# Performance work log

Measured on AMD Instinct MI355X. Metric: run time of the kernel, lower is better.

## Reference

```python
import jax, jax.numpy as jnp
import numpy as np

B, S, D = 2, 2048, 4096
NH, NKV = 32, 8
HD = D // NH          # 128
NREP = NH // NKV      # 4
SCALE = HD ** -0.5


def setup_inputs() -> dict:
    key = jax.random.key(0)
    kx, kq, kk, kv, ko = jax.random.split(key, 5)
    s = 0.02
    return {
        "x": jax.random.normal(kx, (B, S, D), dtype=jnp.float32),
        "wq": jax.random.normal(kq, (D, NH * HD), dtype=jnp.float32) * s,
        "wk": jax.random.normal(kk, (D, NKV * HD), dtype=jnp.float32) * s,
        "wv": jax.random.normal(kv, (D, NKV * HD), dtype=jnp.float32) * s,
        "wo": jax.random.normal(ko, (NH * HD, D), dtype=jnp.float32) * s,
    }


def reference(x, wq, wk, wv, wo):
    b, s, _ = x.shape
    q = (x @ wq).reshape(b, s, NH, HD)    # b s h d
    k = (x @ wk).reshape(b, s, NKV, HD)   # b s kv d
    v = (x @ wv).reshape(b, s, NKV, HD)
    # GQA: repeat kv heads to match query heads
    k = jnp.repeat(k, NREP, axis=2)       # b s h d
    v = jnp.repeat(v, NREP, axis=2)
    scores = jnp.einsum("bihd,bjhd->bhij", q, k) * SCALE  # b h i j
    causal = jnp.tril(jnp.ones((s, s), dtype=bool))
    scores = jnp.where(causal, scores, jnp.finfo(scores.dtype).min)
    attn = jax.nn.softmax(scores, axis=-1)
    out = jnp.einsum("bhij,bjhd->bihd", attn, v)          # b s h d
    out = out.reshape(b, s, NH * HD)
    return out @ wo
```

## Files before the change

kernel.cpp:

```cpp
#include <hip/hip_runtime.h>
#include <cstdint>
#include <cstddef>

typedef __bf16 bf16x8 __attribute__((ext_vector_type(8)));
typedef float  f32x4  __attribute__((ext_vector_type(4)));
typedef unsigned short u16;

#define SCALE_F 0.08838834764831845f
#define QSCALE_F (0.08838834764831845f * 1.4426950408889634f)

__device__ __forceinline__ u16 f2bf(float f) {
  unsigned int u = __builtin_bit_cast(unsigned int, f);
  u += 0x7fffu + ((u >> 16) & 1u);
  return (u16)(u >> 16);
}

__device__ __forceinline__ unsigned cvt_pk_bf16(float lo, float hi) {
  unsigned r;
  asm("v_cvt_pk_bf16_f32 %0, %1, %2" : "=v"(r) : "v"(lo), "v"(hi));
  return r;
}

__device__ __forceinline__ void load_lds16(const void* g, void* l) {
  __builtin_amdgcn_global_load_lds((const __attribute__((address_space(1))) void*)g,
                                   (__attribute__((address_space(3))) void*)l,
                                   16, 0, 0);
}

__global__ __launch_bounds__(256) void prep_all(const float* __restrict__ x,
                                                const float* __restrict__ wq,
                                                const float* __restrict__ wk,
                                                const float* __restrict__ wv,
                                                const float* __restrict__ wo,
                                                u16* __restrict__ xb,
                                                u16* __restrict__ wqkvT,
                                                u16* __restrict__ woT) {
  __shared__ float tile[64][33];
  const int tid = threadIdx.x;
  int blk = blockIdx.x;
  if (blk < 2048) {
    int idx = blk * 256 + tid;
    const int n4 = 4096 * 4096 / 4;
    for (; idx < n4; idx += 2048 * 256) {
      float4 v = ((const float4*)x)[idx];
      uint2 pk;
      pk.x = (unsigned)f2bf(v.x) | ((unsigned)f2bf(v.y) << 16);
      pk.y = (unsigned)f2bf(v.z) | ((unsigned)f2bf(v.w) << 16);
      ((uint2*)xb)[idx] = pk;
    }
    return;
  }
  blk -= 2048;
  const float* in; u16* out; long C; int nbx; float scale;
  if (blk < 8192)       { in = wq; out = wqkvT;                            C = 4096; nbx = 128; scale = QSCALE_F; }
  else if (blk < 10240) { blk -= 8192;  in = wk; out = wqkvT + (size_t)4096 * 4096; C = 1024; nbx = 32; scale = 1.f; }
  else if (blk < 12288) { blk -= 10240; in = wv; out = wqkvT + (size_t)5120 * 4096; C = 1024; nbx = 32; scale = 1.f; }
  else                  { blk -= 12288; in = wo; out = woT;                C = 4096; nbx = 128; scale = 1.f; }
  const long R = 4096;
  const long c0 = (long)(blk % nbx) * 32, r0 = (long)(blk / nbx) * 64;
  {
    const int tx = tid & 31, ty = tid >> 5;
#pragma unroll
    for (int i = 0; i < 8; i++)
      tile[ty + i * 8][tx] = in[(r0 + ty + i * 8) * C + c0 + tx];
  }
  __syncthreads();
  {
    const int tx = tid & 31, cy = tid >> 5;
#pragma unroll
    for (int i = 0; i < 4; i++) {
      int col = cy + i * 8;
      unsigned val = (unsigned)f2bf(tile[2 * tx][col] * scale) |
                     ((unsigned)f2bf(tile[2 * tx + 1][col] * scale) << 16);
      *(unsigned*)&out[(c0 + col) * R + r0 + 2 * tx] = val;
    }
  }
}

__global__ __launch_bounds__(256) void transpose_u16(const u16* __restrict__ in,
                                                     u16* __restrict__ out,
                                                     int R, int C, int ldi, int ldo) {
  __shared__ u16 tile[32][33];
  const int tx = threadIdx.x, ty = threadIdx.y;
  const long c0 = (long)blockIdx.x * 32, r0 = (long)blockIdx.y * 32;
#pragma unroll
  for (int i = 0; i < 4; i++)
    tile[ty + i * 8][tx] = in[(r0 + ty + i * 8) * (long)ldi + c0 + tx];
  __syncthreads();
#pragma unroll
  for (int i = 0; i < 4; i++)
    out[(c0 + ty + i * 8) * (long)ldo + r0 + tx] = tile[tx][ty + i * 8];
}

#define STGA(db, ks, KC) { int kc_ = (KC) < K ? (KC) : 0; \
    load_lds16(gA0 + kc_, &SA[db][ks][s0 * 8]); \
    load_lds16(gA1 + kc_, &SA[db][ks][s1 * 8]); }
#define STGB(db, ks, KC) { int kc_ = (KC) < K ? (KC) : 0; \
    load_lds16(gB0 + kc_, &SB[db][ks][s0 * 8]); \
    load_lds16(gB1 + kc_, &SB[db][ks][s1 * 8]); }

#define PH(MBc, AU, BU, DBn, KSn, MBn, AN, RDB, BN_, STG, DOVM) { \
    STG; \
    if (DOVM) asm volatile("s_waitcnt vmcnt(8)"); \
    __builtin_amdgcn_s_barrier(); \
    _Pragma("unroll") for (int mm = 0; mm < 4; mm++) \
      AN[mm] = *(const bf16x8*)(&SA[DBn][KSn][aoff + (MBn + mm) * 512]); \
    if (RDB) { \
      _Pragma("unroll") for (int n = 0; n < 4; n++) \
        BN_[n] = *(const bf16x8*)(&SB[DBn][KSn][boff + n * 512]); \
    } \
    __builtin_amdgcn_s_setprio(1); \
    _Pragma("unroll") for (int mm = 0; mm < 4; mm++) \
      _Pragma("unroll") for (int n = 0; n < 4; n++) \
        acc[MBc + mm][n] = __builtin_amdgcn_mfma_f32_16x16x32_bf16(AU[mm], BU[n], acc[MBc + mm][n], 0, 0, 0); \
    __builtin_amdgcn_s_setprio(0); \
  }

template <int BF16_OUT>
__device__ __forceinline__ void gemm_body(const u16* __restrict__ A,
                                          const u16* __restrict__ Bt,
                                          void* __restrict__ Cv,
                                          int M, int N, int K, int NBX) {
  __shared__ u16 SA[2][2][8192];
  __shared__ u16 SB[2][2][8192];
  const int tid = threadIdx.x;
  const int lane = tid & 63;
  const int g = lane >> 4, r16 = lane & 15;
  const int wid = tid >> 6;
  const int wm = wid >> 2, wn = wid & 3;

  const int cpx = gridDim.x >> 3;
  const int lin = (blockIdx.x & 7) * cpx + (blockIdx.x >> 3);
  const long bm = (long)(lin / NBX) * 256;
  const long bn = (long)(lin % NBX) * 256;

  const int s0 = tid, s1 = 512 + tid;
  const int rp0 = s0 >> 3, ci0 = (s0 & 7) ^ (rp0 & 7);
  const int rp1 = s1 >> 3, ci1 = (s1 & 7) ^ (rp1 & 7);
  const long gr0 = rp0 * 2 + (ci0 >> 2), gc0 = (ci0 & 3) * 8;
  const long gr1 = rp1 * 2 + (ci1 >> 2), gc1 = (ci1 & 3) * 8;
  const u16* gA0 = A + (bm + gr0) * K + gc0;
  const u16* gA1 = A + (bm + gr1) * K + gc1;
  const u16* gB0 = Bt + (bn + gr0) * K + gc0;
  const u16* gB1 = Bt + (bn + gr1) * K + gc1;

  const int rA = wm * 128 + r16;
  const int aoff = (rA >> 1) * 64 + ((((rA & 1) << 2) + g) ^ ((rA >> 1) & 7)) * 8;
  const int rB = wn * 64 + r16;
  const int boff = (rB >> 1) * 64 + ((((rB & 1) << 2) + g) ^ ((rB >> 1) & 7)) * 8;

  f32x4 acc[8][4];
#pragma unroll
  for (int m = 0; m < 8; m++)
#pragma unroll
    for (int n = 0; n < 4; n++)
#pragma unroll
      for (int j = 0; j < 4; j++) acc[m][n][j] = 0.f;

  bf16x8 afrX[4], afrY[4], bfrX[4], bfrY[4];

  STGA(0, 0, 0); STGB(0, 0, 0);
  STGA(0, 1, 32); STGB(0, 1, 32);
  STGA(1, 0, 64); STGB(1, 0, 64);
  __builtin_amdgcn_sched_barrier(0);
  asm volatile("s_waitcnt vmcnt(0)" ::: "memory");
  __builtin_amdgcn_s_barrier();

#pragma unroll
  for (int mm = 0; mm < 4; mm++)
    afrX[mm] = *(const bf16x8*)(&SA[0][0][aoff + mm * 512]);
#pragma unroll
  for (int n = 0; n < 4; n++)
    bfrX[n] = *(const bf16x8*)(&SB[0][0][boff + n * 512]);

  for (int it = 0; it < K / 128; it++) {
    const int t0 = it * 128;
    PH(0, afrX, bfrX, 0, 0, 4, afrY, 0, bfrY, STGA(1, 1, t0 + 96), 0);
    PH(4, afrY, bfrX, 0, 1, 0, afrX, 1, bfrY, STGB(1, 1, t0 + 96), 1);
    PH(0, afrX, bfrY, 0, 1, 4, afrY, 0, bfrX, STGA(0, 0, t0 + 128), 0);
    PH(4, afrY, bfrY, 1, 0, 0, afrX, 1, bfrX, STGB(0, 0, t0 + 128), 1);
    PH(0, afrX, bfrX, 1, 0, 4, afrY, 0, bfrY, STGA(0, 1, t0 + 160), 0);
    PH(4, afrY, bfrX, 1, 1, 0, afrX, 1, bfrY, STGB(0, 1, t0 + 160), 1);
    PH(0, afrX, bfrY, 1, 1, 4, afrY, 0, bfrX, STGA(1, 0, t0 + 192), 0);
    PH(4, afrY, bfrY, 0, 0, 0, afrX, 1, bfrX, STGB(1, 0, t0 + 192), 1);
  }

  const long crow = bm + wm * 128 + g * 4;
  const long ccol = bn + wn * 64 + r16;
  if (BF16_OUT) {
    u16* C = (u16*)Cv;
#pragma unroll
    for (int m = 0; m < 8; m++)
#pragma unroll
      for (int n = 0; n < 4; n++)
#pragma unroll
        for (int j = 0; j < 4; j++)
          C[(crow + m * 16 + j) * (long)N + ccol + n * 16] = f2bf(acc[m][n][j]);
  } else {
    float* C = (float*)Cv;
#pragma unroll
    for (int m = 0; m < 8; m++)
#pragma unroll
      for (int n = 0; n < 4; n++)
#pragma unroll
        for (int j = 0; j < 4; j++)
          C[(crow + m * 16 + j) * (long)N + ccol + n * 16] = acc[m][n][j];
  }
}

__global__ __launch_bounds__(512, 2) void gemm_qkv(const u16* __restrict__ A,
                                                   const u16* __restrict__ Bt,
                                                   void* __restrict__ Cv,
                                                   int M, int N, int K, int NBX) {
  gemm_body<1>(A, Bt, Cv, M, N, K, NBX);
}
__global__ __launch_bounds__(512, 2) void gemm_wo(const u16* __restrict__ A,
                                                  const u16* __restrict__ Bt,
                                                  void* __restrict__ Cv,
                                                  int M, int N, int K, int NBX) {
  gemm_body<0>(A, Bt, Cv, M, N, K, NBX);
}

__global__ __launch_bounds__(512, 4) void attn_fwd(const u16* __restrict__ QK,
                                                   const u16* __restrict__ VT,
                                                   u16* __restrict__ Og) {
  __shared__ u16 Ks[2][64 * 128];
  __shared__ u16 Vs[2][128 * 64];
  __shared__ u16 Ps[8][16 * 64];
  const int tid = threadIdx.x;
  const int lane = tid & 63;
  const int w = tid >> 6;
  const int g = lane >> 4, r16 = lane & 15;

  const int lin = (blockIdx.x & 7) * 64 + (blockIdx.x >> 3);
  const int b = lin >> 8;
  const int rem = lin & 255;
  const int kvh = rem >> 5;
  const int hrep = (rem & 31) >> 3;
  const int qtA = rem & 7;
  const int qtB = 15 - qtA;
  const int h = kvh * 4 + hrep;

  const u16* kcol   = QK + (long)b * 2048 * 6144 + 4096 + kvh * 128;
  const u16* vb_ptr = VT + (long)kvh * 128 * 4096 + (long)b * 2048;
  u16* pw = Ps[w];

  const int nktA = 2 * (qtA + 1);
  const int ntot = 34;

  int qbase = qtA * 128;
  int qlo = qbase + w * 16;
  int qrow = qlo + r16;

  bf16x8 qf[4];
  auto load_q = [&]() {
    const u16* qp = QK + ((long)(b * 2048 + qrow)) * 6144 + h * 128 + g * 8;
#pragma unroll
    for (int kc = 0; kc < 4; kc++) qf[kc] = *(const bf16x8*)(qp + kc * 32);
  };
  load_q();

  f32x4 oacc[8];
  float mrun, lrun;
  auto reinit = [&]() {
#pragma unroll
    for (int dt = 0; dt < 8; dt++)
#pragma unroll
      for (int j = 0; j < 4; j++) oacc[dt][j] = 0.f;
    mrun = -__builtin_inff();
    lrun = 0.f;
  };
  reinit();

  auto finalize = [&]() {
    float li[4];
#pragma unroll
    for (int j = 0; j < 4; j++)
      li[j] = 1.f / __shfl(lrun, (lane & 48) + g * 4 + j);
    u16* op = Og + ((long)(b * 2048 + qbase + w * 16 + g * 4)) * 4096 + h * 128 + r16;
#pragma unroll
    for (int dt = 0; dt < 8; dt++)
#pragma unroll
      for (int j = 0; j < 4; j++)
        op[(long)j * 4096 + dt * 16] = f2bf(oacc[dt][j] * li[j]);
  };

  auto stage = [&](int bf, int kb) {
#pragma unroll
    for (int i = 0; i < 2; i++) {
      int slot = i * 512 + tid;
      int r = slot >> 4, cs = slot & 15;
      int ck = (cs & 8) | ((cs ^ r) & 7);
      load_lds16(kcol + (long)(kb + r) * 6144 + ck * 8, &Ks[bf][slot * 8]);
      int d = slot >> 3, c8 = slot & 7;
      int cv = (c8 ^ d) & 7;
      load_lds16(vb_ptr + (long)d * 4096 + kb + cv * 8, &Vs[bf][slot * 8]);
    }
  };

  stage(0, 0);
  __syncthreads();
  int cur = 0;

  for (int i = 0; i < ntot; i++) {
    if (i == nktA) {
      finalize();
      qbase = qtB * 128;
      qlo = qbase + w * 16;
      qrow = qlo + r16;
      load_q();
      reinit();
    }
    const int kt = (i < nktA) ? i : i - nktA;
    const int kb = kt * 64;
    if (i + 1 < ntot) {
      const int ktn = (i + 1 < nktA) ? i + 1 : i + 1 - nktA;
      stage(cur ^ 1, ktn * 64);
    }

    if (kb <= qlo + 15) {
      const bool masked = (kb + 63 > qlo);

      f32x4 st[4];
#pragma unroll
      for (int t = 0; t < 4; t++)
#pragma unroll
        for (int j = 0; j < 4; j++) st[t][j] = 0.f;
#pragma unroll
      for (int t = 0; t < 4; t++) {
        const int r = t * 16 + r16;
#pragma unroll
        for (int kc = 0; kc < 4; kc++) {
          int c = kc * 4 + g;
          int cz = (c & 8) | ((c ^ r) & 7);
          bf16x8 kf = *(const bf16x8*)(&Ks[cur][r * 128 + cz * 8]);
          st[t] = __builtin_amdgcn_mfma_f32_16x16x32_bf16(kf, qf[kc], st[t], 0, 0, 0);
        }
      }

      float p[4][4];
      float tmax = -__builtin_inff();
#pragma unroll
      for (int t = 0; t < 4; t++)
#pragma unroll
        for (int j = 0; j < 4; j++) {
          float s = st[t][j];
          if (masked) {
            int kv = kb + t * 16 + g * 4 + j;
            s = (kv > qrow) ? -__builtin_inff() : s;
          }
          p[t][j] = s;
          tmax = fmaxf(tmax, s);
        }
      tmax = fmaxf(tmax, __shfl_xor(tmax, 16));
      tmax = fmaxf(tmax, __shfl_xor(tmax, 32));

      if (!__all(tmax <= mrun + 8.f)) {
        const float mnew = fmaxf(mrun, tmax);
        const float esc = exp2f(mrun - mnew);
        float es[4];
#pragma unroll
        for (int j = 0; j < 4; j++) es[j] = __shfl(esc, (lane & 48) + g * 4 + j);
#pragma unroll
        for (int dt = 0; dt < 8; dt++)
#pragma unroll
          for (int j = 0; j < 4; j++) oacc[dt][j] *= es[j];
        lrun *= esc;
        mrun = mnew;
      }
      float psum = 0.f;
#pragma unroll
      for (int t = 0; t < 4; t++)
#pragma unroll
        for (int j = 0; j < 4; j++) {
          float e = exp2f(p[t][j] - mrun);
          p[t][j] = e;
          psum += e;
        }
      psum += __shfl_xor(psum, 16);
      psum += __shfl_xor(psum, 32);
      lrun += psum;

#pragma unroll
      for (int t = 0; t < 4; t++)
#pragma unroll
        for (int pp = 0; pp < 2; pp++) {
          int kvl = t * 16 + g * 4 + pp * 2;
          unsigned val = cvt_pk_bf16(p[t][pp * 2], p[t][pp * 2 + 1]);
          int off = r16 * 128 + ((kvl * 2) ^ ((r16 & 7) << 4));
          *(unsigned int*)((char*)pw + off) = val;
        }

#pragma unroll
      for (int kc2 = 0; kc2 < 2; kc2++) {
        int c = kc2 * 4 + g;
        int cp = c ^ (r16 & 7);
        bf16x8 pa = *(const bf16x8*)(pw + r16 * 64 + cp * 8);
#pragma unroll
        for (int dt = 0; dt < 8; dt++) {
          int d = dt * 16 + r16;
          int cz = c ^ (d & 7);
          bf16x8 vf = *(const bf16x8*)(&Vs[cur][d * 64 + cz * 8]);
          oacc[dt] = __builtin_amdgcn_mfma_f32_16x16x32_bf16(pa, vf, oacc[dt], 0, 0, 0);
        }
      }
    }

    __syncthreads();
    cur ^= 1;
  }

  finalize();
}

extern "C" void kernel_launch(void* const* d_in, const int* in_sizes, int n_in,
                              void* d_out, int out_size, void* d_ws, size_t ws_size,
                              hipStream_t stream) {
  (void)in_sizes; (void)n_in; (void)out_size; (void)ws_size;
  const float* x  = (const float*)d_in[0];
  const float* wq = (const float*)d_in[1];
  const float* wk = (const float*)d_in[2];
  const float* wv = (const float*)d_in[3];
  const float* wo = (const float*)d_in[4];
  float* out = (float*)d_out;

  u16* xb     = (u16*)d_ws;
  u16* wqkvT  = xb    + (size_t)4096 * 4096;
  u16* woT    = wqkvT + (size_t)6144 * 4096;
  u16* qkv    = woT   + (size_t)4096 * 4096;
  u16* vT     = qkv   + (size_t)4096 * 6144;
  u16* attn   = xb;

  prep_all<<<22528, 256, 0, stream>>>(x, wq, wk, wv, wo, xb, wqkvT, woT);

  gemm_qkv<<<384, 512, 0, stream>>>(xb, wqkvT, qkv, 4096, 6144, 4096, 24);
  transpose_u16<<<dim3(32, 128), dim3(32, 8), 0, stream>>>(qkv + 5120, vT, 4096, 1024, 6144, 4096);

  attn_fwd<<<512, 512, 0, stream>>>(qkv, vT, attn);

  gemm_wo<<<256, 512, 0, stream>>>(attn, woT, out, 4096, 4096, 4096, 16);
}
```

Before: 526.4 us.

## Split QKV GEMM into Q GEMM and split-K KV GEMM with reduction

The fused QKV projection launched 384 tiles of 256x256, which is an awkward count on a 256-CU device. It is replaced by a Q GEMM with 256 tiles and a KV GEMM that splits K in two, also giving 256 tiles. The split-K KV GEMM writes fp32 partials into the output buffer as scratch, and a new reduce kernel sums them and converts to bf16. This balances wave quantization across CUs, at the cost of an extra launch and the fp32 partial traffic.

```diff
diff --git a/kernel.cpp b/kernel.cpp
--- a/kernel.cpp
+++ b/kernel.cpp
@@ -33,7 +33,8 @@
                                                 const float* __restrict__ wv,
                                                 const float* __restrict__ wo,
                                                 u16* __restrict__ xb,
-                                                u16* __restrict__ wqkvT,
+                                                u16* __restrict__ wqT,
+                                                u16* __restrict__ wkvT,
                                                 u16* __restrict__ woT) {
   __shared__ float tile[64][33];
   const int tid = threadIdx.x;
@@ -52,10 +53,10 @@
   }
   blk -= 2048;
   const float* in; u16* out; long C; int nbx; float scale;
-  if (blk < 8192)       { in = wq; out = wqkvT;                            C = 4096; nbx = 128; scale = QSCALE_F; }
-  else if (blk < 10240) { blk -= 8192;  in = wk; out = wqkvT + (size_t)4096 * 4096; C = 1024; nbx = 32; scale = 1.f; }
-  else if (blk < 12288) { blk -= 10240; in = wv; out = wqkvT + (size_t)5120 * 4096; C = 1024; nbx = 32; scale = 1.f; }
-  else                  { blk -= 12288; in = wo; out = woT;                C = 4096; nbx = 128; scale = 1.f; }
+  if (blk < 8192)       { in = wq; out = wqT;                           C = 4096; nbx = 128; scale = QSCALE_F; }
+  else if (blk < 10240) { blk -= 8192;  in = wk; out = wkvT;                          C = 1024; nbx = 32; scale = 1.f; }
+  else if (blk < 12288) { blk -= 10240; in = wv; out = wkvT + (size_t)1024 * 4096;    C = 1024; nbx = 32; scale = 1.f; }
+  else                  { blk -= 12288; in = wo; out = woT;                           C = 4096; nbx = 128; scale = 1.f; }
   const long R = 4096;
   const long c0 = (long)(blk % nbx) * 32, r0 = (long)(blk / nbx) * 64;
   {
@@ -90,6 +91,21 @@
 #pragma unroll
   for (int i = 0; i < 4; i++)
     out[(c0 + ty + i * 8) * (long)ldo + r0 + tx] = tile[tx][ty + i * 8];
+}
+
+__global__ __launch_bounds__(256) void reduce_kv(const float* __restrict__ part,
+                                                 u16* __restrict__ kvb, int n4) {
+  int idx = blockIdx.x * 256 + threadIdx.x;
+  const int stride = gridDim.x * 256;
+  const float4* p0 = (const float4*)part;
+  const float4* p1 = (const float4*)(part + (size_t)4096 * 2048);
+  for (; idx < n4; idx += stride) {
+    float4 a = p0[idx], b = p1[idx];
+    uint2 pk;
+    pk.x = (unsigned)f2bf(a.x + b.x) | ((unsigned)f2bf(a.y + b.y) << 16);
+    pk.y = (unsigned)f2bf(a.z + b.z) | ((unsigned)f2bf(a.w + b.w) << 16);
+    ((uint2*)kvb)[idx] = pk;
+  }
 }
 
 #define STGA(db, ks, KC) { int kc_ = (KC) < K ? (KC) : 0; \
@@ -117,10 +133,11 @@
   }
 
 template <int BF16_OUT>
-__device__ __forceinline__ void gemm_body(const u16* __restrict__ A,
+__device__ __forceinline__ void gemm_core(const u16* __restrict__ A,
                                           const u16* __restrict__ Bt,
                                           void* __restrict__ Cv,
-                                          int M, int N, int K, int NBX) {
+                                          long bm, long bn,
+                                          int N, int K, int lda, int ldb) {
   __shared__ u16 SA[2][2][8192];
   __shared__ u16 SB[2][2][8192];
   const int tid = threadIdx.x;
@@ -129,20 +146,15 @@
   const int wid = tid >> 6;
   const int wm = wid >> 2, wn = wid & 3;
 
-  const int cpx = gridDim.x >> 3;
-  const int lin = (blockIdx.x & 7) * cpx + (blockIdx.x >> 3);
-  const long bm = (long)(lin / NBX) * 256;
-  const long bn = (long)(lin % NBX) * 256;
-
   const int s0 = tid, s1 = 512 + tid;
   const int rp0 = s0 >> 3, ci0 = (s0 & 7) ^ (rp0 & 7);
   const int rp1 = s1 >> 3, ci1 = (s1 & 7) ^ (rp1 & 7);
   const long gr0 = rp0 * 2 + (ci0 >> 2), gc0 = (ci0 & 3) * 8;
   const long gr1 = rp1 * 2 + (ci1 >> 2), gc1 = (ci1 & 3) * 8;
-  const u16* gA0 = A + (bm + gr0) * K + gc0;
-  const u16* gA1 = A + (bm + gr1) * K + gc1;
-  const u16* gB0 = Bt + (bn + gr0) * K + gc0;
-  const u16* gB1 = Bt + (bn + gr1) * K + gc1;
+  const u16* gA0 = A + (bm + gr0) * lda + gc0;
+  const u16* gA1 = A + (bm + gr1) * lda + gc1;
+  const u16* gB0 = Bt + (bn + gr0) * ldb + gc0;
+  const u16* gB1 = Bt + (bn + gr1) * ldb + gc1;
 
   const int rA = wm * 128 + r16;
   const int aoff = (rA >> 1) * 64 + ((((rA & 1) << 2) + g) ^ ((rA >> 1) & 7)) * 8;
@@ -208,20 +220,39 @@
   }
 }
 
-__global__ __launch_bounds__(512, 2) void gemm_qkv(const u16* __restrict__ A,
-                                                   const u16* __restrict__ Bt,
-                                                   void* __restrict__ Cv,
-                                                   int M, int N, int K, int NBX) {
-  gemm_body<1>(A, Bt, Cv, M, N, K, NBX);
-}
+__global__ __launch_bounds__(512, 2) void gemm_q(const u16* __restrict__ A,
+                                                 const u16* __restrict__ Bt,
+                                                 void* __restrict__ Cv) {
+  const int cpx = gridDim.x >> 3;
+  const int lin = ((int)blockIdx.x & 7) * cpx + ((int)blockIdx.x >> 3);
+  gemm_core<1>(A, Bt, Cv, (long)(lin / 16) * 256, (long)(lin % 16) * 256,
+               4096, 4096, 4096, 4096);
+}
+
+__global__ __launch_bounds__(512, 2) void gemm_kv(const u16* __restrict__ A,
+                                                  const u16* __restrict__ Bt,
+                                                  float* __restrict__ part) {
+  const int cpx = gridDim.x >> 3;
+  const int lin = ((int)blockIdx.x & 7) * cpx + ((int)blockIdx.x >> 3);
+  const int sk = lin >> 7;
+  const int t = lin & 127;
+  gemm_core<0>(A + sk * 2048, Bt + sk * 2048,
+               part + (size_t)sk * 4096 * 2048,
+               (long)(t >> 3) * 256, (long)(t & 7) * 256,
+               2048, 2048, 4096, 4096);
+}
+
 __global__ __launch_bounds__(512, 2) void gemm_wo(const u16* __restrict__ A,
                                                   const u16* __restrict__ Bt,
-                                                  void* __restrict__ Cv,
-                                                  int M, int N, int K, int NBX) {
-  gemm_body<0>(A, Bt, Cv, M, N, K, NBX);
-}
-
-__global__ __launch_bounds__(512, 4) void attn_fwd(const u16* __restrict__ QK,
+                                                  void* __restrict__ Cv) {
+  const int cpx = gridDim.x >> 3;
+  const int lin = ((int)blockIdx.x & 7) * cpx + ((int)blockIdx.x >> 3);
+  gemm_core<0>(A, Bt, Cv, (long)(lin / 16) * 256, (long)(lin % 16) * 256,
+               4096, 4096, 4096, 4096);
+}
+
+__global__ __launch_bounds__(512, 4) void attn_fwd(const u16* __restrict__ Q,
+                                                   const u16* __restrict__ KV,
                                                    const u16* __restrict__ VT,
                                                    u16* __restrict__ Og) {
   __shared__ u16 Ks[2][64 * 128];
@@ -232,7 +263,7 @@
   const int w = tid >> 6;
   const int g = lane >> 4, r16 = lane & 15;
 
-  const int lin = (blockIdx.x & 7) * 64 + (blockIdx.x >> 3);
+  const int lin = ((int)blockIdx.x & 7) * 64 + ((int)blockIdx.x >> 3);
   const int b = lin >> 8;
   const int rem = lin & 255;
   const int kvh = rem >> 5;
@@ -241,7 +272,7 @@
   const int qtB = 15 - qtA;
   const int h = kvh * 4 + hrep;
 
-  const u16* kcol   = QK + (long)b * 2048 * 6144 + 4096 + kvh * 128;
+  const u16* kcol   = KV + (long)b * 2048 * 2048 + kvh * 128;
   const u16* vb_ptr = VT + (long)kvh * 128 * 4096 + (long)b * 2048;
   u16* pw = Ps[w];
 
@@ -254,7 +285,7 @@
 
   bf16x8 qf[4];
   auto load_q = [&]() {
-    const u16* qp = QK + ((long)(b * 2048 + qrow)) * 6144 + h * 128 + g * 8;
+    const u16* qp = Q + ((long)(b * 2048 + qrow)) * 4096 + h * 128 + g * 8;
 #pragma unroll
     for (int kc = 0; kc < 4; kc++) qf[kc] = *(const bf16x8*)(qp + kc * 32);
   };
@@ -291,7 +322,7 @@
       int slot = i * 512 + tid;
       int r = slot >> 4, cs = slot & 15;
       int ck = (cs & 8) | ((cs ^ r) & 7);
-      load_lds16(kcol + (long)(kb + r) * 6144 + ck * 8, &Ks[bf][slot * 8]);
+      load_lds16(kcol + (long)(kb + r) * 2048 + ck * 8, &Ks[bf][slot * 8]);
       int d = slot >> 3, c8 = slot & 7;
       int cv = (c8 ^ d) & 7;
       load_lds16(vb_ptr + (long)d * 4096 + kb + cv * 8, &Vs[bf][slot * 8]);
@@ -424,19 +455,23 @@
   const float* wo = (const float*)d_in[4];
   float* out = (float*)d_out;
 
-  u16* xb     = (u16*)d_ws;
-  u16* wqkvT  = xb    + (size_t)4096 * 4096;
-  u16* woT    = wqkvT + (size_t)6144 * 4096;
-  u16* qkv    = woT   + (size_t)4096 * 4096;
-  u16* vT     = qkv   + (size_t)4096 * 6144;
-  u16* attn   = xb;
-
-  prep_all<<<22528, 256, 0, stream>>>(x, wq, wk, wv, wo, xb, wqkvT, woT);
-
-  gemm_qkv<<<384, 512, 0, stream>>>(xb, wqkvT, qkv, 4096, 6144, 4096, 24);
-  transpose_u16<<<dim3(32, 128), dim3(32, 8), 0, stream>>>(qkv + 5120, vT, 4096, 1024, 6144, 4096);
-
-  attn_fwd<<<512, 512, 0, stream>>>(qkv, vT, attn);
-
-  gemm_wo<<<256, 512, 0, stream>>>(attn, woT, out, 4096, 4096, 4096, 16);
-}
+  u16* xb    = (u16*)d_ws;
+  u16* wqT   = xb   + (size_t)4096 * 4096;
+  u16* wkvT  = wqT  + (size_t)4096 * 4096;
+  u16* woT   = wkvT + (size_t)2048 * 4096;
+  u16* qb    = woT  + (size_t)4096 * 4096;
+  u16* kvb   = qb   + (size_t)4096 * 4096;
+  u16* vT    = kvb  + (size_t)4096 * 2048;
+  u16* attn  = xb;
+
+  prep_all<<<22528, 256, 0, stream>>>(x, wq, wk, wv, wo, xb, wqT, wkvT, woT);
+
+  gemm_q<<<256, 512, 0, stream>>>(xb, wqT, qb);
+  gemm_kv<<<256, 512, 0, stream>>>(xb, wkvT, out);
+  reduce_kv<<<2048, 256, 0, stream>>>(out, kvb, 4096 * 2048 / 4);
+  transpose_u16<<<dim3(32, 128), dim3(32, 8), 0, stream>>>(kvb + 1024, vT, 4096, 1024, 2048, 4096);
+
+  attn_fwd<<<512, 512, 0, stream>>>(qb, kvb, vT, attn);
+
+  gemm_wo<<<256, 512, 0, stream>>>(attn, woT, out);
+}
```

Measured after the change: 508.5 us. 3.4% less time.
